# Optimization experiments

Measured on AMD Instinct MI355X. Metric: run time of the kernel, lower is better.

The kernel has to match this reference:

```python
import jax, jax.numpy as jnp
import numpy as np

H = 256          # hidden_dim
D = 64           # dim_dynamic
R = 49           # pooler_resolution ** 2
N = 2000         # bs * num_proposals
EPS = 1e-5


def _ln(x, g, b):
    m = jnp.mean(x, axis=-1, keepdims=True)
    v = jnp.mean(jnp.square(x - m), axis=-1, keepdims=True)
    return (x - m) * jax.lax.rsqrt(v + EPS) * g + b


def setup_inputs() -> dict:
    key = jax.random.key(0)
    ks = jax.random.split(key, 6)
    pro_features = jax.random.normal(ks[0], (1, N, H), dtype=jnp.float32)
    roi_features = jax.random.normal(ks[1], (R, N, H), dtype=jnp.float32)
    # dynamic_layer: Linear(H, num_dynamic * H * D) with num_dynamic = 2
    W_dyn = jax.random.normal(ks[2], (H, 2 * H * D), dtype=jnp.float32) * 0.02
    b_dyn = jnp.zeros((2 * H * D,), dtype=jnp.float32)
    # out_layer: Linear(H * R, H)
    W_out = jax.random.normal(ks[3], (H * R, H), dtype=jnp.float32) * 0.02
    b_out = jnp.zeros((H,), dtype=jnp.float32)
    g1 = jnp.ones((D,), dtype=jnp.float32); b1 = jnp.zeros((D,), dtype=jnp.float32)
    g2 = jnp.ones((H,), dtype=jnp.float32); b2 = jnp.zeros((H,), dtype=jnp.float32)
    g3 = jnp.ones((H,), dtype=jnp.float32); b3 = jnp.zeros((H,), dtype=jnp.float32)
    return {"pro_features": pro_features, "roi_features": roi_features,
            "W_dyn": W_dyn, "b_dyn": b_dyn, "W_out": W_out, "b_out": b_out,
            "g1": g1, "b1": b1, "g2": g2, "b2": b2, "g3": g3, "b3": b3}


def reference(pro_features, roi_features, W_dyn, b_dyn, W_out, b_out,
              g1, b1, g2, b2, g3, b3):
    # roi_features: (R, N, H) -> features: (N, R, H)
    feats = jnp.transpose(roi_features, (1, 0, 2))
    # per-instance dynamic parameters: (N, 2*H*D)
    params = pro_features[0] @ W_dyn + b_dyn
    num_params = H * D
    p1 = params[:, :num_params].reshape(-1, H, D)   # (N, H, D)
    p2 = params[:, num_params:].reshape(-1, D, H)   # (N, D, H)
    f = jnp.einsum('nrh,nhd->nrd', feats, p1)       # bmm 1
    f = jax.nn.relu(_ln(f, g1, b1))
    f = jnp.einsum('nrd,ndh->nrh', f, p2)           # bmm 2
    f = jax.nn.relu(_ln(f, g2, b2))
    f = f.reshape(f.shape[0], R * H)                # flatten(1)
    f = jax.nn.relu(_ln(f @ W_out + b_out, g3, b3))
    return f  # (N, H)
```

## Files before the change

kernel.cpp:

```cpp
#include <hip/hip_runtime.h>

typedef unsigned short u16;
typedef __attribute__((ext_vector_type(8))) short short8;
typedef __attribute__((ext_vector_type(4))) float f32x4;

#define N_INST 2000
#define H_DIM 256
#define D_DIM 64
#define R_DIM 49
#define LN_EPS 1e-5f
#define SPLITK 14

__device__ __forceinline__ u16 f2bf(float f) {
  union { float f; unsigned int i; } x; x.f = f;
  unsigned int r = x.i + 0x7fffu + ((x.i >> 16) & 1u);
  return (u16)(r >> 16);
}
__device__ __forceinline__ float bf2f(u16 u) {
  union { unsigned int i; float f; } x; x.i = ((unsigned int)u) << 16; return x.f;
}
__device__ __forceinline__ short8 ld8(const u16* p) {
  return *reinterpret_cast<const short8*>(p);
}
__device__ __forceinline__ short8 pack8(float4 a, float4 b) {
  short8 r;
  r[0] = (short)f2bf(a.x); r[1] = (short)f2bf(a.y);
  r[2] = (short)f2bf(a.z); r[3] = (short)f2bf(a.w);
  r[4] = (short)f2bf(b.x); r[5] = (short)f2bf(b.y);
  r[6] = (short)f2bf(b.z); r[7] = (short)f2bf(b.w);
  return r;
}
__device__ __forceinline__ f32x4 mfma16(short8 a, short8 b, f32x4 c) {
  return __builtin_amdgcn_mfma_f32_16x16x32_bf16(a, b, c, 0, 0, 0);
}
__device__ __forceinline__ void wave_reduce2(float& s, float& s2) {
#pragma unroll
  for (int off = 32; off > 0; off >>= 1) {
    s  += __shfl_down(s, off);
    s2 += __shfl_down(s2, off);
  }
  s = __shfl(s, 0); s2 = __shfl(s2, 0);
}
__device__ __forceinline__ void gload16(const u16* g, u16* l) {
  __builtin_amdgcn_global_load_lds(
      (const __attribute__((address_space(1))) void*)g,
      (__attribute__((address_space(3))) void*)l, 16, 0, 0);
}

__global__ __launch_bounds__(256) void prep_all(
    const float* __restrict__ pro,  u16* __restrict__ proB,
    const float* __restrict__ Wdyn, u16* __restrict__ WdynT,
    const float* __restrict__ Wout, u16* __restrict__ WoutT) {
  __shared__ u16 T[64][65];
  const int tid = threadIdx.x;
  const int wave = tid >> 6, lane = tid & 63;
  const int b = blockIdx.x;
  if (b < 2048) {
    const int half = b >> 10;
    const int bb = b & 1023;
    const int kt = bb >> 8;
    long colbase, rowbase; int rstride;
    if (half == 0) {
      int h = bb & 255;
      colbase = (long)h * 64; rowbase = h; rstride = 256;
    } else {
      int d = bb & 63, hc = (bb >> 6) & 3;
      colbase = 16384L + d * 256 + hc * 64;
      rowbase = 16384L + hc * 4096 + d; rstride = 64;
    }
#pragma unroll
    for (int i = 0; i < 16; ++i) {
      int kk = wave * 16 + i;
      int k = kt * 64 + kk;
      T[kk][lane] = f2bf(Wdyn[(long)k * 32768 + colbase + lane]);
    }
    __syncthreads();
#pragma unroll
    for (int i = 0; i < 16; ++i) {
      int jj = wave * 16 + i;
      long ro = rowbase + (long)jj * rstride;
      WdynT[ro * 256 + kt * 64 + lane] = T[lane][jj];
    }
  } else if (b < 2832) {
    const int b2 = b - 2048;
    const int kt = b2 >> 2, ct = b2 & 3;
#pragma unroll
    for (int i = 0; i < 16; ++i) {
      int kk = wave * 16 + i;
      long k = (long)kt * 64 + kk;
      T[kk][lane] = f2bf(Wout[k * 256 + ct * 64 + lane]);
    }
    __syncthreads();
#pragma unroll
    for (int i = 0; i < 16; ++i) {
      int cc = wave * 16 + i;
      long c = (long)ct * 64 + cc;
      WoutT[c * 12544 + (long)kt * 64 + lane] = T[lane][cc];
    }
  } else {
    const int n4 = 128000;
    for (int i = (b - 2832) * 256 + tid; i < n4; i += 500 * 256) {
      float4 v = ((const float4*)pro)[i];
      u16* op = proB + i * 4;
      op[0] = f2bf(v.x); op[1] = f2bf(v.y); op[2] = f2bf(v.z); op[3] = f2bf(v.w);
    }
  }
}

__global__ __launch_bounds__(512, 1) void gemm256p(
    const u16* __restrict__ A,
    const u16* __restrict__ BT,
    const float* __restrict__ bias,
    u16* __restrict__ C)
{
  union Smem {
    struct { u16 a[2][256 * 32]; u16 b[2][128 * 32]; } s;
    u16 cb[256 * 128];
  };
  __shared__ Smem sm;

  const int tid = threadIdx.x;
  const int wave = tid >> 6, lane = tid & 63;
  const int quad = lane >> 4, l16 = lane & 15;
  const int wm = wave >> 1, wn = wave & 1;
  const int bid = blockIdx.x;
  const int mblk = bid >> 8, nblk = bid & 255;
  const int m0 = mblk * 256, n0 = nblk * 128;

  const int ca = tid & 3;
  const int ra = tid >> 2;
  const int cg = ca ^ ((ra >> 1) & 3);
  int gr0 = m0 + ra;       if (gr0 >= N_INST) gr0 = N_INST - 1;
  int gr1 = m0 + 128 + ra; if (gr1 >= N_INST) gr1 = N_INST - 1;
  const u16* gA0 = A + (long)gr0 * 256 + cg * 8;
  const u16* gA1 = A + (long)gr1 * 256 + cg * 8;
  const u16* gB0 = BT + (long)(n0 + ra) * 256 + cg * 8;

  int fAoff[4], fBoff[4];
#pragma unroll
  for (int i = 0; i < 4; ++i) {
    int rt = wm * 64 + i * 16 + l16;
    fAoff[i] = rt * 32 + (quad ^ ((rt >> 1) & 3)) * 8;
    int ct = wn * 64 + i * 16 + l16;
    fBoff[i] = ct * 32 + (quad ^ ((ct >> 1) & 3)) * 8;
  }

  f32x4 acc[4][4];
#pragma unroll
  for (int mi = 0; mi < 4; ++mi)
#pragma unroll
    for (int ni = 0; ni < 4; ++ni) acc[mi][ni] = f32x4{0.f, 0.f, 0.f, 0.f};

  gload16(gA0, &sm.s.a[0][tid * 8]);
  gload16(gA1, &sm.s.a[0][(tid + 512) * 8]);
  gload16(gB0, &sm.s.b[0][tid * 8]);

  for (int ks = 0; ks < 8; ++ks) {
    const int cur = ks & 1, nxt = cur ^ 1;
    __syncthreads();
    if (ks + 1 < 8) {
      const int ko = (ks + 1) * 32;
      gload16(gA0 + ko, &sm.s.a[nxt][tid * 8]);
      gload16(gA1 + ko, &sm.s.a[nxt][(tid + 512) * 8]);
      gload16(gB0 + ko, &sm.s.b[nxt][tid * 8]);
    }
    short8 av[4], bv[4];
#pragma unroll
    for (int i = 0; i < 4; ++i) {
      av[i] = ld8(&sm.s.a[cur][fAoff[i]]);
      bv[i] = ld8(&sm.s.b[cur][fBoff[i]]);
    }
#pragma unroll
    for (int mi = 0; mi < 4; ++mi)
#pragma unroll
      for (int ni = 0; ni < 4; ++ni)
        acc[mi][ni] = mfma16(av[mi], bv[ni], acc[mi][ni]);
  }

  float bvv[4];
#pragma unroll
  for (int ni = 0; ni < 4; ++ni) {
    int col = n0 + wn * 64 + ni * 16 + l16;
    int bi = (col < 16384) ? (((col & 255) << 6) + (col >> 8))
                           : (16384 + ((col & 63) << 8) + ((col >> 6) & 255));
    bvv[ni] = bias[bi];
  }
  __syncthreads();
#pragma unroll
  for (int mi = 0; mi < 4; ++mi)
#pragma unroll
    for (int ni = 0; ni < 4; ++ni)
#pragma unroll
      for (int i = 0; i < 4; ++i) {
        int row = wm * 64 + mi * 16 + quad * 4 + i;
        int col = wn * 64 + ni * 16 + l16;
        sm.cb[row * 128 + col] = f2bf(acc[mi][ni][i] + bvv[ni]);
      }
  __syncthreads();
#pragma unroll
  for (int j = 0; j < 8; ++j) {
    int lin = j * 4096 + tid * 8;
    int row = lin >> 7, col = lin & 127;
    int grow = m0 + row;
    if (grow < N_INST)
      *reinterpret_cast<short8*>(C + (long)grow * 32768 + n0 + col) =
          ld8(&sm.cb[lin]);
  }
}

__global__ __launch_bounds__(256, 3) void gemm128(
    const u16* __restrict__ A, int lda, int M,
    const u16* __restrict__ BT, int ldbt,
    void* __restrict__ Cout, int ldc, long c_stride_s,
    int ksteps, int n_blocks)
{
  struct Smem { u16 a[2][128 * 32]; u16 b[2][128 * 32]; };
  __shared__ Smem sm;

  const int tid = threadIdx.x;
  const int wave = tid >> 6, lane = tid & 63;
  const int quad = lane >> 4, l16 = lane & 15;
  const int wm = wave >> 1, wn = wave & 1;
  const int bid = blockIdx.x;
  const int mblk = bid / n_blocks, nblk = bid - mblk * n_blocks;
  const int m0 = mblk * 128, n0 = nblk * 128;
  const int s = blockIdx.y;
  const int kb = s * ksteps * 32;

  const int cl = tid & 3;
  const int r0 = tid >> 2, r1 = 64 + (tid >> 2);
  const int cg0 = cl ^ ((r0 >> 1) & 3);
  const int cg1 = cl ^ ((r1 >> 1) & 3);
  int ga0 = m0 + r0; if (ga0 >= M) ga0 = M - 1;
  int ga1 = m0 + r1; if (ga1 >= M) ga1 = M - 1;
  const u16* gA0 = A + (long)ga0 * lda + kb + cg0 * 8;
  const u16* gA1 = A + (long)ga1 * lda + kb + cg1 * 8;
  const u16* gB0 = BT + (long)(n0 + r0) * ldbt + kb + cg0 * 8;
  const u16* gB1 = BT + (long)(n0 + r1) * ldbt + kb + cg1 * 8;

  int fAoff[4], fBoff[4];
#pragma unroll
  for (int i = 0; i < 4; ++i) {
    int rt = wm * 64 + i * 16 + l16;
    fAoff[i] = rt * 32 + (quad ^ ((rt >> 1) & 3)) * 8;
    int ct = wn * 64 + i * 16 + l16;
    fBoff[i] = ct * 32 + (quad ^ ((ct >> 1) & 3)) * 8;
  }

  f32x4 acc[4][4];
#pragma unroll
  for (int mi = 0; mi < 4; ++mi)
#pragma unroll
    for (int ni = 0; ni < 4; ++ni) acc[mi][ni] = f32x4{0.f, 0.f, 0.f, 0.f};

  gload16(gA0, &sm.a[0][tid * 8]);
  gload16(gA1, &sm.a[0][(tid + 256) * 8]);
  gload16(gB0, &sm.b[0][tid * 8]);
  gload16(gB1, &sm.b[0][(tid + 256) * 8]);

  for (int ks = 0; ks < ksteps; ++ks) {
    const int cur = ks & 1, nxt = cur ^ 1;
    __syncthreads();
    if (ks + 1 < ksteps) {
      const int ko = (ks + 1) * 32;
      gload16(gA0 + ko, &sm.a[nxt][tid * 8]);
      gload16(gA1 + ko, &sm.a[nxt][(tid + 256) * 8]);
      gload16(gB0 + ko, &sm.b[nxt][tid * 8]);
      gload16(gB1 + ko, &sm.b[nxt][(tid + 256) * 8]);
    }
    short8 av[4], bv[4];
#pragma unroll
    for (int i = 0; i < 4; ++i) {
      av[i] = ld8(&sm.a[cur][fAoff[i]]);
      bv[i] = ld8(&sm.b[cur][fBoff[i]]);
    }
#pragma unroll
    for (int mi = 0; mi < 4; ++mi)
#pragma unroll
      for (int ni = 0; ni < 4; ++ni)
        acc[mi][ni] = mfma16(av[mi], bv[ni], acc[mi][ni]);
  }

  float* Cp = (float*)Cout + (long)s * c_stride_s;
#pragma unroll
  for (int mi = 0; mi < 4; ++mi)
#pragma unroll
    for (int ni = 0; ni < 4; ++ni) {
      int col = n0 + wn * 64 + ni * 16 + l16;
#pragma unroll
      for (int i = 0; i < 4; ++i) {
        int row = m0 + wm * 64 + mi * 16 + quad * 4 + i;
        if (row < M) Cp[(long)row * ldc + col] = acc[mi][ni][i];
      }
    }
}

__global__ __launch_bounds__(256, 4) void bmm12_ln(
    const float* __restrict__ roi,
    const u16* __restrict__ P12,
    const float* __restrict__ g1, const float* __restrict__ b1,
    const float* __restrict__ g2, const float* __restrict__ b2,
    u16* __restrict__ f2n)
{
  __shared__ __align__(16) u16 p1b[16384];
  __shared__ __align__(16) u16 f1b[4096];
  const int n = blockIdx.x;
  const int tid = threadIdx.x;
  const int wave = tid >> 6, lane = tid & 63;
  const int quad = lane >> 4, l16 = lane & 15;
  const int wstripe = wave * 16;

  const u16* P1n = P12 + (long)n * 32768;
#pragma unroll
  for (int j = 0; j < 8; ++j) {
    int lc = j * 256 + tid;
    int d = lc >> 5, c = lc & 31;
    int cg = (c & 24) | ((c & 7) ^ (d & 7));
    gload16(P1n + d * 256 + cg * 8, &p1b[lc * 8]);
  }
  int r = wstripe + l16;
  int rr = (r < R_DIM) ? r : 0;
  const float* Arow = roi + ((long)rr * N_INST + n) * H_DIM + quad * 8;
  short8 sa[8];
#pragma unroll
  for (int ks = 0; ks < 8; ++ks) {
    float4 va = ((const float4*)(Arow + ks * 32))[0];
    float4 vb = ((const float4*)(Arow + ks * 32))[1];
    sa[ks] = pack8(va, vb);
  }
  const u16* P2n = P12 + (long)n * 32768 + 16384;
  short8 pf[4][2];
#pragma unroll
  for (int hs = 0; hs < 4; ++hs)
#pragma unroll
    for (int ks = 0; ks < 2; ++ks) {
      int h = wave * 64 + hs * 16 + l16;
      pf[hs][ks] = ld8(P2n + h * 64 + (ks * 4 + quad) * 8);
    }
  float gv1[4], bv1[4];
#pragma unroll
  for (int sub = 0; sub < 4; ++sub) {
    gv1[sub] = g1[sub * 16 + l16]; bv1[sub] = b1[sub * 16 + l16];
  }
  __syncthreads();

  f32x4 acc1[4];
#pragma unroll
  for (int i = 0; i < 4; ++i) acc1[i] = f32x4{0.f, 0.f, 0.f, 0.f};
#pragma unroll
  for (int ks = 0; ks < 8; ++ks) {
#pragma unroll
    for (int sub = 0; sub < 4; ++sub) {
      int d = sub * 16 + l16;
      int q = ks * 4 + quad;
      int c = (q & 24) | ((q & 7) ^ (d & 7));
      acc1[sub] = mfma16(sa[ks], ld8(&p1b[d * 256 + c * 8]), acc1[sub]);
    }
  }

  {
    float s1[4], s2[4];
#pragma unroll
    for (int i = 0; i < 4; ++i) {
      s1[i] = 0.f; s2[i] = 0.f;
#pragma unroll
      for (int sub = 0; sub < 4; ++sub) {
        float v = acc1[sub][i]; s1[i] += v; s2[i] += v * v;
      }
    }
#pragma unroll
    for (int m = 1; m < 16; m <<= 1)
#pragma unroll
      for (int i = 0; i < 4; ++i) {
        s1[i] += __shfl_xor(s1[i], m, 16);
        s2[i] += __shfl_xor(s2[i], m, 16);
      }
#pragma unroll
    for (int i = 0; i < 4; ++i) {
      float mean = s1[i] * (1.f / 64.f);
      float var = s2[i] * (1.f / 64.f) - mean * mean;
      float rs = rsqrtf(var + LN_EPS);
      int row = wstripe + quad * 4 + i;
#pragma unroll
      for (int sub = 0; sub < 4; ++sub) {
        float y = fmaxf((acc1[sub][i] - mean) * rs * gv1[sub] + bv1[sub], 0.f);
        int kc = (sub * 2 + (l16 >> 3)) ^ (row & 7);
        f1b[row * 64 + kc * 8 + (l16 & 7)] = f2bf(y);
      }
    }
  }
  __syncthreads();

  f32x4 acc2[4][4];
#pragma unroll
  for (int rs = 0; rs < 4; ++rs)
#pragma unroll
    for (int hs = 0; hs < 4; ++hs) acc2[rs][hs] = f32x4{0.f, 0.f, 0.f, 0.f};
#pragma unroll
  for (int ks = 0; ks < 2; ++ks) {
#pragma unroll
    for (int rs = 0; rs < 4; ++rs) {
      int row = rs * 16 + l16;
      int c2 = (ks * 4 + quad) ^ (row & 7);
      short8 af = ld8(&f1b[row * 64 + c2 * 8]);
#pragma unroll
      for (int hs = 0; hs < 4; ++hs)
        acc2[rs][hs] = mfma16(af, pf[hs][ks], acc2[rs][hs]);
    }
  }

  float s1[4][4], s2[4][4];
#pragma unroll
  for (int rs = 0; rs < 4; ++rs)
#pragma unroll
    for (int i = 0; i < 4; ++i) {
      float a = 0.f, b = 0.f;
#pragma unroll
      for (int hs = 0; hs < 4; ++hs) {
        float v = acc2[rs][hs][i]; a += v; b += v * v;
      }
      s1[rs][i] = a; s2[rs][i] = b;
    }
#pragma unroll
  for (int m = 1; m < 16; m <<= 1)
#pragma unroll
    for (int rs = 0; rs < 4; ++rs)
#pragma unroll
      for (int i = 0; i < 4; ++i) {
        s1[rs][i] += __shfl_xor(s1[rs][i], m, 16);
        s2[rs][i] += __shfl_xor(s2[rs][i], m, 16);
      }
  float2* lnst = reinterpret_cast<float2*>(&p1b[14336]);
  if (l16 == 0) {
#pragma unroll
    for (int rs = 0; rs < 4; ++rs)
#pragma unroll
      for (int i = 0; i < 4; ++i) {
        int row = rs * 16 + quad * 4 + i;
        lnst[row * 4 + wave] = float2{s1[rs][i], s2[rs][i]};
      }
  }
  __syncthreads();

#pragma unroll
  for (int rs = 0; rs < 4; ++rs)
#pragma unroll
    for (int i = 0; i < 4; ++i) {
      int row = rs * 16 + quad * 4 + i;
      f32x4 qa = *reinterpret_cast<const f32x4*>(&lnst[row * 4]);
      f32x4 qb = *reinterpret_cast<const f32x4*>(&lnst[row * 4 + 2]);
      float S1 = qa[0] + qa[2] + qb[0] + qb[2];
      float S2 = qa[1] + qa[3] + qb[1] + qb[3];
      float mean = S1 * (1.f / 256.f);
      float var = S2 * (1.f / 256.f) - mean * mean;
      float rsq = rsqrtf(var + LN_EPS);
      if (row < R_DIM) {
#pragma unroll
        for (int hs = 0; hs < 4; ++hs)
          p1b[row * 264 + wave * 64 + hs * 16 + l16] =
              f2bf((acc2[rs][hs][i] - mean) * rsq);
      }
    }
  __syncthreads();

  u16* f2out = f2n + (long)n * (R_DIM * H_DIM);
  for (int t = tid; t < R_DIM * 32; t += 256) {
    int row = t >> 5, c = t & 31;
    short8 z8 = ld8(&p1b[row * 264 + c * 8]);
    const float4* gp = (const float4*)(g2 + c * 8);
    const float4* bp = (const float4*)(b2 + c * 8);
    float4 ga = gp[0], gb = gp[1], ba = bp[0], bb = bp[1];
    short8 y;
    y[0] = (short)f2bf(fmaxf(bf2f((u16)z8[0]) * ga.x + ba.x, 0.f));
    y[1] = (short)f2bf(fmaxf(bf2f((u16)z8[1]) * ga.y + ba.y, 0.f));
    y[2] = (short)f2bf(fmaxf(bf2f((u16)z8[2]) * ga.z + ba.z, 0.f));
    y[3] = (short)f2bf(fmaxf(bf2f((u16)z8[3]) * ga.w + ba.w, 0.f));
    y[4] = (short)f2bf(fmaxf(bf2f((u16)z8[4]) * gb.x + bb.x, 0.f));
    y[5] = (short)f2bf(fmaxf(bf2f((u16)z8[5]) * gb.y + bb.y, 0.f));
    y[6] = (short)f2bf(fmaxf(bf2f((u16)z8[6]) * gb.z + bb.z, 0.f));
    y[7] = (short)f2bf(fmaxf(bf2f((u16)z8[7]) * gb.w + bb.w, 0.f));
    *reinterpret_cast<short8*>(f2out + row * 256 + c * 8) = y;
  }
}

__global__ __launch_bounds__(64) void ln3_k(
    const float* __restrict__ partial,
    const float* __restrict__ b_out,
    const float* __restrict__ g3, const float* __restrict__ b3,
    float* __restrict__ out)
{
  const int n = blockIdx.x;
  const int lane = threadIdx.x;
  float x[4], sv = 0.f, s2 = 0.f;
#pragma unroll
  for (int j = 0; j < 4; ++j) {
    int h = lane + 64 * j;
    float v = b_out[h];
#pragma unroll
    for (int ss = 0; ss < SPLITK; ++ss)
      v += partial[((long)ss * N_INST + n) * H_DIM + h];
    x[j] = v; sv += v; s2 += v * v;
  }
  wave_reduce2(sv, s2);
  float mean = sv * (1.f / 256.f);
  float var = s2 * (1.f / 256.f) - mean * mean;
  float rs = rsqrtf(var + LN_EPS);
#pragma unroll
  for (int j = 0; j < 4; ++j) {
    int h = lane + 64 * j;
    float y = fmaxf((x[j] - mean) * rs * g3[h] + b3[h], 0.f);
    out[(long)n * H_DIM + h] = y;
  }
}

extern "C" void kernel_launch(void* const* d_in, const int* in_sizes, int n_in,
                              void* d_out, int out_size, void* d_ws, size_t ws_size,
                              hipStream_t stream) {
  const float* pro  = (const float*)d_in[0];
  const float* roi  = (const float*)d_in[1];
  const float* Wdyn = (const float*)d_in[2];
  const float* bdyn = (const float*)d_in[3];
  const float* Wout = (const float*)d_in[4];
  const float* bout = (const float*)d_in[5];
  const float* g1 = (const float*)d_in[6];
  const float* b1 = (const float*)d_in[7];
  const float* g2 = (const float*)d_in[8];
  const float* b2 = (const float*)d_in[9];
  const float* g3 = (const float*)d_in[10];
  const float* b3 = (const float*)d_in[11];
  float* out = (float*)d_out;

  char* ws = (char*)d_ws;
  u16* proB  = (u16*)ws;
  u16* WdynT = (u16*)(ws + 1024000);
  u16* WoutT = (u16*)(ws + 17801216);
  u16* P12   = (u16*)(ws + 24223744);
  u16* f2n   = (u16*)(ws + 155295744);
  float* partial = (float*)(ws + 24223744);

  dim3 blk(256);

  prep_all<<<dim3(3332), blk, 0, stream>>>(pro, proB, Wdyn, WdynT, Wout, WoutT);

  gemm256p<<<dim3(2048), dim3(512), 0, stream>>>(proB, WdynT, bdyn, P12);

  bmm12_ln<<<dim3(N_INST), blk, 0, stream>>>(roi, P12, g1, b1, g2, b2, f2n);

  gemm128<<<dim3(16 * 2, SPLITK), blk, 0, stream>>>(
      f2n, R_DIM * H_DIM, N_INST, WoutT, R_DIM * H_DIM,
      (void*)partial, H_DIM, (long)N_INST * H_DIM, 28, 2);

  ln3_k<<<dim3(N_INST), dim3(64), 0, stream>>>(partial, bout, g3, b3, out);
}
```

Measured before the change: 333.3 us.

## Load full-K tiles into LDS once for the dynamic-param GEMM

The per-instance parameter GEMM (K=256) is rewritten to load entire 128x256 A and B tiles into shared memory in a single pass with an XOR swizzle, then run all eight k-steps without intermediate barriers. The block shape changes from 256x128 with 512 threads to 128x128 with 256 threads, doubling the grid to 4096 blocks. The goal is to remove the per-k-step synchronisation and double-buffer pipeline overhead. In exchange, each block uses 128KB of LDS, so occupancy is limited to one block per CU and the global loads no longer overlap with MFMA work.

```diff
diff --git a/kernel.cpp b/kernel.cpp
--- a/kernel.cpp
+++ b/kernel.cpp
@@ -107,76 +107,37 @@
   }
 }
 
-__global__ __launch_bounds__(512, 1) void gemm256p(
+__global__ __launch_bounds__(256, 1) void gemm_pk(
     const u16* __restrict__ A,
     const u16* __restrict__ BT,
     const float* __restrict__ bias,
     u16* __restrict__ C)
 {
-  union Smem {
-    struct { u16 a[2][256 * 32]; u16 b[2][128 * 32]; } s;
-    u16 cb[256 * 128];
-  };
-  __shared__ Smem sm;
-
+  __shared__ __align__(16) u16 al[128 * 256];
+  __shared__ __align__(16) u16 bl[128 * 256];
   const int tid = threadIdx.x;
   const int wave = tid >> 6, lane = tid & 63;
   const int quad = lane >> 4, l16 = lane & 15;
   const int wm = wave >> 1, wn = wave & 1;
   const int bid = blockIdx.x;
   const int mblk = bid >> 8, nblk = bid & 255;
-  const int m0 = mblk * 256, n0 = nblk * 128;
-
-  const int ca = tid & 3;
-  const int ra = tid >> 2;
-  const int cg = ca ^ ((ra >> 1) & 3);
-  int gr0 = m0 + ra;       if (gr0 >= N_INST) gr0 = N_INST - 1;
-  int gr1 = m0 + 128 + ra; if (gr1 >= N_INST) gr1 = N_INST - 1;
-  const u16* gA0 = A + (long)gr0 * 256 + cg * 8;
-  const u16* gA1 = A + (long)gr1 * 256 + cg * 8;
-  const u16* gB0 = BT + (long)(n0 + ra) * 256 + cg * 8;
-
-  int fAoff[4], fBoff[4];
-#pragma unroll
-  for (int i = 0; i < 4; ++i) {
-    int rt = wm * 64 + i * 16 + l16;
-    fAoff[i] = rt * 32 + (quad ^ ((rt >> 1) & 3)) * 8;
-    int ct = wn * 64 + i * 16 + l16;
-    fBoff[i] = ct * 32 + (quad ^ ((ct >> 1) & 3)) * 8;
-  }
-
-  f32x4 acc[4][4];
-#pragma unroll
-  for (int mi = 0; mi < 4; ++mi)
-#pragma unroll
-    for (int ni = 0; ni < 4; ++ni) acc[mi][ni] = f32x4{0.f, 0.f, 0.f, 0.f};
-
-  gload16(gA0, &sm.s.a[0][tid * 8]);
-  gload16(gA1, &sm.s.a[0][(tid + 512) * 8]);
-  gload16(gB0, &sm.s.b[0][tid * 8]);
-
-  for (int ks = 0; ks < 8; ++ks) {
-    const int cur = ks & 1, nxt = cur ^ 1;
-    __syncthreads();
-    if (ks + 1 < 8) {
-      const int ko = (ks + 1) * 32;
-      gload16(gA0 + ko, &sm.s.a[nxt][tid * 8]);
-      gload16(gA1 + ko, &sm.s.a[nxt][(tid + 512) * 8]);
-      gload16(gB0 + ko, &sm.s.b[nxt][tid * 8]);
-    }
-    short8 av[4], bv[4];
-#pragma unroll
-    for (int i = 0; i < 4; ++i) {
-      av[i] = ld8(&sm.s.a[cur][fAoff[i]]);
-      bv[i] = ld8(&sm.s.b[cur][fBoff[i]]);
-    }
-#pragma unroll
-    for (int mi = 0; mi < 4; ++mi)
-#pragma unroll
-      for (int ni = 0; ni < 4; ++ni)
-        acc[mi][ni] = mfma16(av[mi], bv[ni], acc[mi][ni]);
-  }
-
+  const int m0 = mblk * 128, n0 = nblk * 128;
+
+#pragma unroll
+  for (int j = 0; j < 16; ++j) {
+    int lc = j * 256 + tid;
+    int row = lc >> 5, c = lc & 31;
+    int cg = (c & 24) | ((c & 7) ^ (row & 7));
+    int ga = m0 + row; if (ga >= N_INST) ga = N_INST - 1;
+    gload16(A + (long)ga * 256 + cg * 8, &al[lc * 8]);
+  }
+#pragma unroll
+  for (int j = 0; j < 16; ++j) {
+    int lc = j * 256 + tid;
+    int row = lc >> 5, c = lc & 31;
+    int cg = (c & 24) | ((c & 7) ^ (row & 7));
+    gload16(BT + (long)(n0 + row) * 256 + cg * 8, &bl[lc * 8]);
+  }
   float bvv[4];
 #pragma unroll
   for (int ni = 0; ni < 4; ++ni) {
@@ -186,6 +147,34 @@
     bvv[ni] = bias[bi];
   }
   __syncthreads();
+
+  f32x4 acc[4][4];
+#pragma unroll
+  for (int mi = 0; mi < 4; ++mi)
+#pragma unroll
+    for (int ni = 0; ni < 4; ++ni) acc[mi][ni] = f32x4{0.f, 0.f, 0.f, 0.f};
+
+#pragma unroll
+  for (int ks = 0; ks < 8; ++ks) {
+    short8 av[4], bv[4];
+#pragma unroll
+    for (int i = 0; i < 4; ++i) {
+      int q = ks * 4 + quad;
+      int rt = wm * 64 + i * 16 + l16;
+      int cA = (q & 24) | ((q & 7) ^ (rt & 7));
+      av[i] = ld8(&al[rt * 256 + cA * 8]);
+      int ct = wn * 64 + i * 16 + l16;
+      int cB = (q & 24) | ((q & 7) ^ (ct & 7));
+      bv[i] = ld8(&bl[ct * 256 + cB * 8]);
+    }
+#pragma unroll
+    for (int mi = 0; mi < 4; ++mi)
+#pragma unroll
+      for (int ni = 0; ni < 4; ++ni)
+        acc[mi][ni] = mfma16(av[mi], bv[ni], acc[mi][ni]);
+  }
+
+  __syncthreads();
 #pragma unroll
   for (int mi = 0; mi < 4; ++mi)
 #pragma unroll
@@ -194,17 +183,17 @@
       for (int i = 0; i < 4; ++i) {
         int row = wm * 64 + mi * 16 + quad * 4 + i;
         int col = wn * 64 + ni * 16 + l16;
-        sm.cb[row * 128 + col] = f2bf(acc[mi][ni][i] + bvv[ni]);
+        al[row * 128 + col] = f2bf(acc[mi][ni][i] + bvv[ni]);
       }
   __syncthreads();
 #pragma unroll
   for (int j = 0; j < 8; ++j) {
-    int lin = j * 4096 + tid * 8;
+    int lin = j * 2048 + tid * 8;
     int row = lin >> 7, col = lin & 127;
     int grow = m0 + row;
     if (grow < N_INST)
       *reinterpret_cast<short8*>(C + (long)grow * 32768 + n0 + col) =
-          ld8(&sm.cb[lin]);
+          ld8(&al[lin]);
   }
 }
 
@@ -542,7 +531,7 @@
 
   prep_all<<<dim3(3332), blk, 0, stream>>>(pro, proB, Wdyn, WdynT, Wout, WoutT);
 
-  gemm256p<<<dim3(2048), dim3(512), 0, stream>>>(proB, WdynT, bdyn, P12);
+  gemm_pk<<<dim3(4096), blk, 0, stream>>>(proB, WdynT, bdyn, P12);
 
   bmm12_ln<<<dim3(N_INST), blk, 0, stream>>>(roi, P12, g1, b1, g2, b2, f2n);
 
```

Measured after the change: 360.5 us. 8.2% more time.
